# Optimization experiments

Hardware: AMD Instinct MI355X
Metric: run time of the kernel (lower is better)

## Reference

```python
import jax, jax.numpy as jnp
import numpy as np

B, NPG, K, H, G, L = 8, 128, 64, 600, 50, 6
N = B * NPG
CUTOFF = 10.0
BOX = 20.0
NUM_Z = 100


def setup_inputs() -> dict:
    key = jax.random.key(0)
    ks = jax.random.split(key, 16)
    s = 0.05
    z = jax.random.randint(ks[0], (N,), 0, 85)
    pos = jax.random.uniform(ks[1], (N, 3), dtype=jnp.float32) * BOX
    # weights stored as [in, out] (transposed torch Linear) so x @ w applies directly
    inp = {
        "z": z,
        "pos": pos,
        "embedding": jax.random.normal(ks[2], (NUM_Z, H), jnp.float32) * s,
        "mlp_w1": jax.random.normal(ks[3], (L, G, H), jnp.float32) * s,
        "mlp_b1": jnp.zeros((L, H), jnp.float32),
        "mlp_w2": jax.random.normal(ks[4], (L, H, H), jnp.float32) * s,
        "mlp_b2": jnp.zeros((L, H), jnp.float32),
        "lin1_w": jax.random.normal(ks[5], (L, H, H), jnp.float32) * s,  # CFConv lin1, no bias
        "lin2_w": jax.random.normal(ks[6], (L, H, H), jnp.float32) * s,
        "lin2_b": jnp.zeros((L, H), jnp.float32),
        "int_lin_w": jax.random.normal(ks[7], (L, H, H), jnp.float32) * s,
        "int_lin_b": jnp.zeros((L, H), jnp.float32),
        "pool_w": jax.random.normal(ks[8], (H, H), jnp.float32) * s,
        "pool_b": jnp.zeros((H,), jnp.float32),
    }
    return inp


def _ssp(x):
    # shifted softplus used by SchNet
    return jax.nn.softplus(x) - jnp.log(2.0)


def _build_graph(pos):
    # radius graph within each of the B graphs, capped at K neighbors per node
    posg = pos.reshape(B, NPG, 3)
    diff = posg[:, :, None, :] - posg[:, None, :, :]          # [B,n,n,3]
    dist2 = jnp.sum(diff * diff, axis=-1)                     # [B,n,n]
    eye = jnp.eye(NPG, dtype=bool)
    ok = (dist2 <= CUTOFF * CUTOFF) & (~eye)[None]
    neg = jnp.where(ok, -dist2, -jnp.inf)
    vals, idx = jax.lax.top_k(neg, K)                         # nearest K in-radius
    valid = jnp.isfinite(vals)                                # [B,n,K]
    nbr = idx + (jnp.arange(B) * NPG)[:, None, None]          # global node ids
    # recompute distances from gathered positions (differentiable, safe at masked slots)
    pos_nbr = pos[nbr.reshape(-1)].reshape(B, NPG, K, 3)
    dvec = posg[:, :, None, :] - pos_nbr
    dsq = jnp.sum(dvec * dvec, axis=-1)
    d = jnp.sqrt(jnp.where(valid, dsq, 1.0))
    d = jnp.where(valid, d, 0.0)                              # [B,n,K]
    return nbr, d, valid.astype(pos.dtype)


def reference(pos, embedding, mlp_w1, mlp_b1, mlp_w2, mlp_b2, lin1_w, lin2_w,
              lin2_b, int_lin_w, int_lin_b, pool_w, pool_b, z):
    nbr, d, valid = _build_graph(pos)
    nbr_flat = nbr.reshape(-1)

    # Gaussian smearing
    offs = jnp.linspace(0.0, CUTOFF, G)
    coeff = -0.5 / (offs[1] - offs[0]) ** 2
    edge_attr = jnp.exp(coeff * (d[..., None] - offs) ** 2)   # [B,n,K,G]
    # cosine cutoff, zero for invalid (padded) edges
    C = 0.5 * (jnp.cos(d * jnp.pi / CUTOFF) + 1.0) * valid    # [B,n,K]

    h = embedding[z]                                          # [N,H]
    for l in range(L):
        Wf = _ssp(edge_attr @ mlp_w1[l] + mlp_b1[l]) @ mlp_w2[l] + mlp_b2[l]
        Wf = Wf * C[..., None]                                # [B,n,K,H]
        x1 = h @ lin1_w[l]                                    # [N,H]
        xj = x1[nbr_flat].reshape(B, NPG, K, H)               # gather neighbors
        msg = jnp.sum(xj * Wf, axis=2).reshape(N, H)          # aggregate (add)
        m = msg @ lin2_w[l] + lin2_b[l]
        m = _ssp(m)
        m = m @ int_lin_w[l] + int_lin_b[l]
        h = h + m

    pooled = h.reshape(B, NPG, H).mean(axis=1)                # mean pool per graph
    return pooled @ pool_w + pool_b                           # [B, emb_dim]
```

## Files before the change

### kernel.cpp

```cpp
#include <hip/hip_runtime.h>
#include <cmath>

#define NB   8
#define NPG  128
#define NN   1024
#define KNB  64
#define HD   600
#define GG   50
#define LL   6
#define WROW 640
#define WCOL 640
#define NKNOT 1024

typedef __attribute__((ext_vector_type(8))) short short8;
typedef __attribute__((ext_vector_type(4))) float f32x4;

#define GLOAD16(gsrc, ldst) \
  __builtin_amdgcn_global_load_lds( \
      (const __attribute__((address_space(1))) void*)(gsrc), \
      (__attribute__((address_space(3))) void*)(ldst), 16, 0, 0)

__device__ __forceinline__ short f2b(float f) {
  union { float f; unsigned u; } v; v.f = f;
  unsigned u = v.u;
  u += 0x7fffu + ((u >> 16) & 1u);
  return (short)(u >> 16);
}

__device__ __forceinline__ float b2f(unsigned us) {
  union { unsigned u; float f; } v; v.u = us << 16; return v.f;
}

__device__ __forceinline__ float ssp_fast(float x) {
  return fmaxf(x, 0.0f) + __logf(1.0f + __expf(-fabsf(x))) - 0.69314718055994531f;
}

__global__ __launch_bounds__(256) void prolog_k(
    const float* __restrict__ pos, int* __restrict__ nbr,
    float* __restrict__ dist, float* __restrict__ cval,
    const float* __restrict__ w1, short* __restrict__ basis, short* __restrict__ w1b,
    const float* __restrict__ l1w, const float* __restrict__ l2w,
    const float* __restrict__ ilw, const float* __restrict__ w2,
    short* __restrict__ nwall,
    const int* __restrict__ z, const float* __restrict__ emb,
    float* __restrict__ h, short* __restrict__ hb, float* __restrict__ pooled) {
  int bid = blockIdx.x;
  int tid = threadIdx.x;
  if (bid < 512) {
#pragma clang fp contract(off)
    __shared__ float d2s[2][128];
    __shared__ int scnt[2];
    int sub = tid >> 7;
    int j = tid & 127;
    int i = bid*2 + sub;
    int li = i & 127;
    int base = i - li;
    if (j == 0) scnt[sub] = 0;
    float px = pos[3*i], py = pos[3*i+1], pz = pos[3*i+2];
    int gj = base + j;
    float dx = px - pos[3*gj], dy = py - pos[3*gj+1], dz = pz - pos[3*gj+2];
    float d2 = dx*dx + dy*dy + dz*dz;
    bool valid = (j != li) && (d2 <= 100.0f);
    d2s[sub][j] = valid ? d2 : 3.0e38f;
    __syncthreads();
    if (valid) {
      atomicAdd(&scnt[sub], 1);
      int rank = 0;
      for (int j2 = 0; j2 < 128; ++j2) {
        float o = d2s[sub][j2];
        rank += (o < d2 || (o == d2 && j2 < j)) ? 1 : 0;
      }
      if (rank < KNB) {
        int e = i*KNB + rank;
        nbr[e] = gj;
        float d = sqrtf(d2);
        dist[e] = d;
        cval[e] = 0.5f * (cosf(d * 0.31415926535897931f) + 1.0f);
      }
    }
    __syncthreads();
    int cnt = scnt[sub]; if (cnt > KNB) cnt = KNB;
    if (j < KNB && j >= cnt) {
      int e = i*KNB + j;
      nbr[e] = i; dist[e] = 0.0f; cval[e] = 0.0f;
    }
  } else if (bid < 1728) {
    int idx = (bid - 512)*256 + tid;
    if (idx < NKNOT*64) {
      int i = idx >> 6, g = idx & 63;
      float v = 0.0f;
      if (g < GG) {
        const float step = 10.0f/49.0f;
        const float coeff = -0.5f/(step*step);
        float d = (float)i * (10.0f/(float)(NKNOT-1));
        float dd = d - step*(float)g;
        v = __expf(coeff*dd*dd);
      }
      basis[idx] = f2b(v);
    } else {
      int r = idx - NKNOT*64;
      if (r < LL*WROW*64) {
        int l = r / (WROW*64); int rem = r - l*WROW*64;
        int n = rem >> 6, k = rem & 63;
        float v = (n < HD && k < GG) ? w1[(size_t)l*GG*HD + (size_t)k*HD + n] : 0.0f;
        w1b[r] = f2b(v);
      }
    }
  } else if (bid < 4128) {
    __shared__ float T[64][65];
    int r = bid - 1728;
    int w = r / 100; int rem = r - w*100;
    int ny = rem / 10, nz = rem - ny*10;
    int kind = w / 6, l = w - kind*6;
    const float* s = (kind == 0) ? l1w : (kind == 1) ? l2w : (kind == 2) ? ilw : w2;
    s += (size_t)l*360000;
    int n0 = ny*64, k0 = nz*64;
    int ta = tid & 63, tb = tid >> 6;
    #pragma unroll
    for (int p = 0; p < 16; ++p) {
      int k = k0 + p*4 + tb;
      int n = n0 + ta;
      T[p*4 + tb][ta] = (k < HD && n < HD) ? s[(size_t)k*HD + n] : 0.0f;
    }
    __syncthreads();
    #pragma unroll
    for (int p = 0; p < 16; ++p) {
      int n = n0 + p*4 + tb;
      int k = k0 + ta;
      if (k < WCOL)
        nwall[(size_t)w*WROW*WCOL + (size_t)n*WCOL + k] = f2b(T[ta][p*4 + tb]);
    }
  } else {
    int i = bid - 4128;
    int zi = z[i];
    for (int j = tid; j < WCOL; j += 256) {
      float v = (j < HD) ? emb[(size_t)zi*HD + j] : 0.0f;
      if (j < HD) h[(size_t)i*HD + j] = v;
      hb[(size_t)i*WCOL + j] = f2b(v);
    }
    if (i < NB) {
      for (int c = tid; c < HD; c += 256) pooled[(size_t)i*HD + c] = 0.0f;
    }
  }
}

__global__ __launch_bounds__(256) void tabA_k(const short* __restrict__ basis,
    const short* __restrict__ w1b, const float* __restrict__ b1all,
    short* __restrict__ ttab_all) {
  const int MT = NKNOT/128;
  int l = blockIdx.x / MT;
  int mb = blockIdx.x - l*MT;
  const short* Bw = w1b + (size_t)l*WROW*64;
  short* outb = ttab_all + (size_t)l*NKNOT*WCOL;
  __shared__ __align__(16) short As[128*40];
  __shared__ __align__(16) short Bs[128*40];
  int tid = threadIdx.x;
  int lane = tid & 63, wv = tid >> 6;
  int wr = wv >> 1, wc = wv & 1;
  int col = lane & 15, quad = lane >> 4;
  int m0 = mb * 128;
  int n0 = blockIdx.y * 128;
  f32x4 acc[4][4] = {};
  for (int k0 = 0; k0 < 64; k0 += 32) {
    #pragma unroll
    for (int rep = 0; rep < 2; ++rep) {
      int s = tid + rep*256;
      int row = s >> 2, seg = s & 3;
      *(short8*)&As[row*40 + seg*8] =
          *(const short8*)(basis + (size_t)(m0 + row)*64 + k0 + seg*8);
      *(short8*)&Bs[row*40 + seg*8] =
          *(const short8*)(Bw + (size_t)(n0 + row)*64 + k0 + seg*8);
    }
    __syncthreads();
    short8 af[4], bf[4];
    #pragma unroll
    for (int mt = 0; mt < 4; ++mt)
      af[mt] = *(const short8*)&As[(wr*64 + mt*16 + col)*40 + quad*8];
    #pragma unroll
    for (int jt = 0; jt < 4; ++jt)
      bf[jt] = *(const short8*)&Bs[(wc*64 + jt*16 + col)*40 + quad*8];
    #pragma unroll
    for (int mt = 0; mt < 4; ++mt)
      #pragma unroll
      for (int jt = 0; jt < 4; ++jt)
        acc[mt][jt] = __builtin_amdgcn_mfma_f32_16x16x32_bf16(af[mt], bf[jt], acc[mt][jt], 0, 0, 0);
    __syncthreads();
  }
  #pragma unroll
  for (int jt = 0; jt < 4; ++jt) {
    int j = n0 + wc*64 + jt*16 + col;
    if (j >= WCOL) continue;
    float bj = (j < HD) ? b1all[(size_t)l*HD + j] : 0.0f;
    #pragma unroll
    for (int mt = 0; mt < 4; ++mt)
      #pragma unroll
      for (int r = 0; r < 4; ++r) {
        int row = m0 + wr*64 + mt*16 + quad*4 + r;
        short v = (j < HD) ? f2b(ssp_fast(acc[mt][jt][r] + bj)) : (short)0;
        outb[(size_t)row*WCOL + j] = v;
      }
  }
}

__global__ __launch_bounds__(256) void tabB_k(const short* __restrict__ ttab_all,
    const short* __restrict__ nwall, const float* __restrict__ b2all,
    short* __restrict__ wtab_b) {
  const int MT = NKNOT/128;
  int l = blockIdx.x / MT;
  int mb = blockIdx.x - l*MT;
  const short* A  = ttab_all + (size_t)l*NKNOT*WCOL;
  const short* Bw = nwall + (size_t)(18 + l)*WROW*WCOL;
  short* P = wtab_b + (size_t)l*NKNOT*HD;
  __shared__ __align__(16) short As[128*40];
  __shared__ __align__(16) short Bs[128*40];
  int tid = threadIdx.x;
  int lane = tid & 63, wv = tid >> 6;
  int wr = wv >> 1, wc = wv & 1;
  int col = lane & 15, quad = lane >> 4;
  int m0 = mb * 128;
  int n0 = blockIdx.y * 128;
  f32x4 acc[4][4] = {};
  for (int k0 = 0; k0 < WCOL; k0 += 32) {
    #pragma unroll
    for (int rep = 0; rep < 2; ++rep) {
      int s = tid + rep*256;
      int row = s >> 2, seg = s & 3;
      *(short8*)&As[row*40 + seg*8] =
          *(const short8*)(A + (size_t)(m0 + row)*WCOL + k0 + seg*8);
      *(short8*)&Bs[row*40 + seg*8] =
          *(const short8*)(Bw + (size_t)(n0 + row)*WCOL + k0 + seg*8);
    }
    __syncthreads();
    short8 af[4], bf[4];
    #pragma unroll
    for (int mt = 0; mt < 4; ++mt)
      af[mt] = *(const short8*)&As[(wr*64 + mt*16 + col)*40 + quad*8];
    #pragma unroll
    for (int jt = 0; jt < 4; ++jt)
      bf[jt] = *(const short8*)&Bs[(wc*64 + jt*16 + col)*40 + quad*8];
    #pragma unroll
    for (int mt = 0; mt < 4; ++mt)
      #pragma unroll
      for (int jt = 0; jt < 4; ++jt)
        acc[mt][jt] = __builtin_amdgcn_mfma_f32_16x16x32_bf16(af[mt], bf[jt], acc[mt][jt], 0, 0, 0);
    __syncthreads();
  }
  #pragma unroll
  for (int jt = 0; jt < 4; ++jt) {
    int j = n0 + wc*64 + jt*16 + col;
    if (j >= HD) continue;
    float bj = b2all[(size_t)l*HD + j];
    #pragma unroll
    for (int mt = 0; mt < 4; ++mt)
      #pragma unroll
      for (int r = 0; r < 4; ++r) {
        int row = m0 + wr*64 + mt*16 + quad*4 + r;
        P[(size_t)row*HD + j] = f2b(acc[mt][jt][r] + bj);
      }
  }
}

__global__ __launch_bounds__(320) void gather_k(const short* __restrict__ tabb,
    const float* __restrict__ cval, const int* __restrict__ nbr,
    const float* __restrict__ dist, const short* __restrict__ x1b,
    short* __restrict__ msgb) {
  __shared__ float cvs[64];
  __shared__ int nbs[64];
  __shared__ int tix[64];
  __shared__ float tfr[64];
  int node = blockIdx.x, tid = threadIdx.x;
  if (tid < 64) {
    int e = node*KNB + tid;
    cvs[tid] = cval[e];
    nbs[tid] = nbr[e];
    float u = dist[e] * ((float)(NKNOT-1)/10.0f);
    int i = (int)u;
    if (i > NKNOT-2) i = NKNOT-2;
    tix[tid] = i;
    tfr[tid] = u - (float)i;
  }
  __syncthreads();
  int j = tid*2;
  if (j >= HD) {
    *(unsigned*)&msgb[(size_t)node*WCOL + j] = 0u;
    return;
  }
  float s0 = 0.f, s1 = 0.f;
  #pragma unroll 4
  for (int e = 0; e < KNB; ++e) {
    float Ce = cvs[e];
    if (Ce == 0.0f) continue;
    const short* w0 = tabb + (size_t)tix[e]*HD + j;
    float f = tfr[e];
    unsigned wa = *(const unsigned*)w0;
    unsigned wb = *(const unsigned*)(w0 + HD);
    unsigned xv = *(const unsigned*)(x1b + (size_t)nbs[e]*WCOL + j);
    float a0 = b2f(wa & 0xffffu), a1 = b2f(wa >> 16);
    float b0 = b2f(wb & 0xffffu), b1 = b2f(wb >> 16);
    float x0 = b2f(xv & 0xffffu), x1v = b2f(xv >> 16);
    s0 += Ce * (a0 + f*(b0 - a0)) * x0;
    s1 += Ce * (a1 + f*(b1 - a1)) * x1v;
  }
  unsigned pack = (unsigned)(unsigned short)f2b(s0) |
                  ((unsigned)(unsigned short)f2b(s1) << 16);
  *(unsigned*)&msgb[(size_t)node*WCOL + j] = pack;
}

template<int MODE>
__global__ __launch_bounds__(512) void gemm_node_k(
    const short* __restrict__ A, const short* __restrict__ Bw,
    const float* __restrict__ bias,
    short* __restrict__ outb, float* __restrict__ hacc, float* __restrict__ pooled) {
  __shared__ __align__(16) short As[2][2][32*64];
  __shared__ __align__(16) short Bs[2][2][64*64];
  __shared__ __align__(16) float red[2][256*8];
  int tid = threadIdx.x;
  int g = tid >> 8;
  int t = tid & 255;
  int lane = t & 63, wv = t >> 6;
  int col = lane & 15, quad = lane >> 4;
  int m0 = blockIdx.x * 32;
  int n0 = blockIdx.y * 64;
  const int kb = g * 320;
  int a_gi = wv*64 + lane;
  int a_row = a_gi >> 3;
  int a_gc = (a_gi & 7) ^ (a_row & 7);
  const short* a_src = A + (size_t)(m0 + a_row)*WCOL + kb + a_gc*8;
  int b_gi0 = wv*128 + lane;
  int b_row0 = b_gi0 >> 3;
  int b_gc0 = (b_gi0 & 7) ^ (b_row0 & 7);
  const short* b_src0 = Bw + (size_t)(n0 + b_row0)*WCOL + kb + b_gc0*8;
  int b_gi1 = b_gi0 + 64;
  int b_row1 = b_gi1 >> 3;
  int b_gc1 = (b_gi1 & 7) ^ (b_row1 & 7);
  const short* b_src1 = Bw + (size_t)(n0 + b_row1)*WCOL + kb + b_gc1*8;
  short* a_dst[2]  = { &As[g][0][a_gi*8],  &As[g][1][a_gi*8] };
  short* b_dst0[2] = { &Bs[g][0][b_gi0*8], &Bs[g][1][b_gi0*8] };
  short* b_dst1[2] = { &Bs[g][0][b_gi1*8], &Bs[g][1][b_gi1*8] };
  GLOAD16(a_src, a_dst[0]);
  GLOAD16(b_src0, b_dst0[0]);
  GLOAD16(b_src1, b_dst1[0]);
  __syncthreads();
  f32x4 acc[2] = {};
  #pragma unroll
  for (int kk = 0; kk < 5; ++kk) {
    const int cur = kk & 1, nxt = cur ^ 1;
    if (kk < 4) {
      GLOAD16(a_src + (kk+1)*64, a_dst[nxt]);
      GLOAD16(b_src0 + (kk+1)*64, b_dst0[nxt]);
      GLOAD16(b_src1 + (kk+1)*64, b_dst1[nxt]);
    }
    #pragma unroll
    for (int kh = 0; kh < 2; ++kh) {
      int brow = wv*16 + col;
      int bgr = brow*8 + ((kh*4 + quad) ^ (brow & 7));
      short8 bf = *(const short8*)&Bs[g][cur][bgr*8];
      #pragma unroll
      for (int mt = 0; mt < 2; ++mt) {
        int arow = mt*16 + col;
        int agr = arow*8 + ((kh*4 + quad) ^ (arow & 7));
        short8 af = *(const short8*)&As[g][cur][agr*8];
        acc[mt] = __builtin_amdgcn_mfma_f32_16x16x32_bf16(af, bf, acc[mt], 0, 0, 0);
      }
    }
    __syncthreads();
  }
  #pragma unroll
  for (int mt = 0; mt < 2; ++mt)
    *(f32x4*)&red[g][(t*2 + mt)*4] = acc[mt];
  __syncthreads();
  const int mt = g;
  f32x4 v = *(const f32x4*)&red[0][(t*2 + mt)*4];
  v += *(const f32x4*)&red[1][(t*2 + mt)*4];
  int j = n0 + wv*16 + col;
  if (MODE == 0) {
    #pragma unroll
    for (int r = 0; r < 4; ++r) {
      int row = m0 + mt*16 + quad*4 + r;
      outb[(size_t)row*WCOL + j] = (j < HD) ? f2b(v[r]) : (short)0;
    }
  } else if (MODE == 1) {
    float bj = (j < HD) ? bias[j] : 0.0f;
    #pragma unroll
    for (int r = 0; r < 4; ++r) {
      int row = m0 + mt*16 + quad*4 + r;
      outb[(size_t)row*WCOL + j] = (j < HD) ? f2b(ssp_fast(v[r] + bj)) : (short)0;
    }
  } else {
    float psum = 0.0f;
    #pragma unroll
    for (int r = 0; r < 4; ++r) {
      int row = m0 + mt*16 + quad*4 + r;
      if (j < HD) {
        float nv = hacc[(size_t)row*HD + j] + v[r] + bias[j];
        hacc[(size_t)row*HD + j] = nv;
        outb[(size_t)row*WCOL + j] = f2b(nv);
        psum += nv;
      } else {
        outb[(size_t)row*WCOL + j] = 0;
      }
    }
    if (MODE == 3 && j < HD) {
      int b = m0 >> 7;
      atomicAdd(&pooled[(size_t)b*HD + j], psum * (1.0f/128.0f));
    }
  }
}

__global__ __launch_bounds__(256) void pool_out_k(const float* __restrict__ pooled,
    const float* __restrict__ pw, const float* __restrict__ pb,
    float* __restrict__ out) {
  __shared__ float red[4][64];
  int b = blockIdx.y;
  int tid = threadIdx.x;
  int jl = tid & 63, q = tid >> 6;
  int j = blockIdx.x*64 + jl;
  float s = 0.0f;
  if (j < HD) {
    int c0 = q*150, c1 = c0 + 150;
    for (int c = c0; c < c1; ++c)
      s += pooled[(size_t)b*HD + c] * pw[(size_t)c*HD + j];
  }
  red[q][jl] = s;
  __syncthreads();
  if (q == 0 && j < HD)
    out[(size_t)b*HD + j] = red[0][jl] + red[1][jl] + red[2][jl] + red[3][jl] + pb[j];
}

extern "C" void kernel_launch(void* const* d_in, const int* in_sizes, int n_in,
                              void* d_out, int out_size, void* d_ws, size_t ws_size,
                              hipStream_t stream) {
  const int*   z    = (const int*)d_in[0];
  const float* pos  = (const float*)d_in[1];
  const float* emb  = (const float*)d_in[2];
  const float* w1   = (const float*)d_in[3];
  const float* b1   = (const float*)d_in[4];
  const float* w2   = (const float*)d_in[5];
  const float* b2   = (const float*)d_in[6];
  const float* l1w  = (const float*)d_in[7];
  const float* l2w  = (const float*)d_in[8];
  const float* l2b  = (const float*)d_in[9];
  const float* ilw  = (const float*)d_in[10];
  const float* ilb  = (const float*)d_in[11];
  const float* pw   = (const float*)d_in[12];
  const float* pb   = (const float*)d_in[13];
  float* ws = (float*)d_ws;
  int*   nbr   = (int*)ws;
  float* cv    = ws + 65536;
  float* dist  = ws + 131072;
  float* pooled= ws + 196608;
  float* h     = ws + 204800;
  short* h_b   = (short*)(ws + 819200);
  short* msg_b = (short*)(ws + 1146880);
  short* mtmp_b= (short*)(ws + 1474560);
  short* x1_b  = (short*)(ws + 1802240);
  short* basis = (short*)(ws + 2129920);
  short* ttab  = (short*)(ws + 2162688);
  short* wtab_b= (short*)(ws + 4128768);
  short* w1b   = (short*)(ws + 5971968);
  short* nwall = (short*)(ws + 6094848);
  float* out   = (float*)d_out;

  const size_t WSZ = (size_t)WROW*WCOL;

  prolog_k<<<5152, 256, 0, stream>>>(pos, nbr, dist, cv,
      w1, basis, w1b, l1w, l2w, ilw, w2, nwall, z, emb, h, h_b, pooled);
  tabA_k<<<dim3(LL*(NKNOT/128), 5), 256, 0, stream>>>(basis, w1b, b1, ttab);
  tabB_k<<<dim3(LL*(NKNOT/128), 5), 256, 0, stream>>>(ttab, nwall, b2, wtab_b);

  dim3 gn(32, 10);
  for (int l = 0; l < LL; ++l) {
    gemm_node_k<0><<<gn, 512, 0, stream>>>(h_b, nwall + (size_t)(0*6 + l)*WSZ,
        nullptr, x1_b, nullptr, nullptr);
    gather_k<<<NN, 320, 0, stream>>>(wtab_b + (size_t)l*NKNOT*HD, cv, nbr, dist, x1_b, msg_b);
    gemm_node_k<1><<<gn, 512, 0, stream>>>(msg_b, nwall + (size_t)(1*6 + l)*WSZ,
        l2b + (size_t)l*HD, mtmp_b, nullptr, nullptr);
    if (l < LL-1)
      gemm_node_k<2><<<gn, 512, 0, stream>>>(mtmp_b, nwall + (size_t)(2*6 + l)*WSZ,
          ilb + (size_t)l*HD, h_b, h, nullptr);
    else
      gemm_node_k<3><<<gn, 512, 0, stream>>>(mtmp_b, nwall + (size_t)(2*6 + l)*WSZ,
          ilb + (size_t)l*HD, h_b, h, pooled);
  }
  pool_out_k<<<dim3(10, NB), 256, 0, stream>>>(pooled, pw, pb, out);
}
```

Measured before the change: 408.6 us.

## Double-buffer tabB GEMM tiles via direct global-to-LDS loads with XOR swizzle

The table-building GEMM kernel now stages its A and B tiles with asynchronous global_load_lds into two LDS buffers. The next K-slice is prefetched while MFMAs run on the current one, which is meant to hide global load latency behind compute. Padded rows are replaced by an XOR-swizzled 32-short layout to avoid LDS bank conflicts without the padding. This doubles LDS use and relies on correct wait/barrier placement for the async copies.

```diff
diff --git a/kernel.cpp b/kernel.cpp
--- a/kernel.cpp
+++ b/kernel.cpp
@@ -211,33 +211,49 @@
   const short* A  = ttab_all + (size_t)l*NKNOT*WCOL;
   const short* Bw = nwall + (size_t)(18 + l)*WROW*WCOL;
   short* P = wtab_b + (size_t)l*NKNOT*HD;
-  __shared__ __align__(16) short As[128*40];
-  __shared__ __align__(16) short Bs[128*40];
+  __shared__ __align__(16) short As[2][128*32];
+  __shared__ __align__(16) short Bs[2][128*32];
   int tid = threadIdx.x;
   int lane = tid & 63, wv = tid >> 6;
   int wr = wv >> 1, wc = wv & 1;
   int col = lane & 15, quad = lane >> 4;
   int m0 = mb * 128;
   int n0 = blockIdx.y * 128;
+  int g0 = tid, g1 = tid + 256;
+  int r0 = g0 >> 2, s0 = (g0 & 3) ^ (r0 & 3);
+  int r1 = g1 >> 2, s1 = (g1 & 3) ^ (r1 & 3);
+  const short* a_s0 = A  + (size_t)(m0 + r0)*WCOL + s0*8;
+  const short* a_s1 = A  + (size_t)(m0 + r1)*WCOL + s1*8;
+  const short* b_s0 = Bw + (size_t)(n0 + r0)*WCOL + s0*8;
+  const short* b_s1 = Bw + (size_t)(n0 + r1)*WCOL + s1*8;
+  GLOAD16(a_s0, &As[0][g0*8]);
+  GLOAD16(a_s1, &As[0][g1*8]);
+  GLOAD16(b_s0, &Bs[0][g0*8]);
+  GLOAD16(b_s1, &Bs[0][g1*8]);
+  __syncthreads();
   f32x4 acc[4][4] = {};
-  for (int k0 = 0; k0 < WCOL; k0 += 32) {
-    #pragma unroll
-    for (int rep = 0; rep < 2; ++rep) {
-      int s = tid + rep*256;
-      int row = s >> 2, seg = s & 3;
-      *(short8*)&As[row*40 + seg*8] =
-          *(const short8*)(A + (size_t)(m0 + row)*WCOL + k0 + seg*8);
-      *(short8*)&Bs[row*40 + seg*8] =
-          *(const short8*)(Bw + (size_t)(n0 + row)*WCOL + k0 + seg*8);
-    }
-    __syncthreads();
+  for (int kk = 0; kk < 20; ++kk) {
+    int cur = kk & 1, nxt = cur ^ 1;
+    if (kk < 19) {
+      int k0 = (kk + 1)*32;
+      GLOAD16(a_s0 + k0, &As[nxt][g0*8]);
+      GLOAD16(a_s1 + k0, &As[nxt][g1*8]);
+      GLOAD16(b_s0 + k0, &Bs[nxt][g0*8]);
+      GLOAD16(b_s1 + k0, &Bs[nxt][g1*8]);
+    }
     short8 af[4], bf[4];
     #pragma unroll
-    for (int mt = 0; mt < 4; ++mt)
-      af[mt] = *(const short8*)&As[(wr*64 + mt*16 + col)*40 + quad*8];
-    #pragma unroll
-    for (int jt = 0; jt < 4; ++jt)
-      bf[jt] = *(const short8*)&Bs[(wc*64 + jt*16 + col)*40 + quad*8];
+    for (int mt = 0; mt < 4; ++mt) {
+      int ar = wr*64 + mt*16 + col;
+      int agr = ar*4 + (quad ^ (ar & 3));
+      af[mt] = *(const short8*)&As[cur][agr*8];
+    }
+    #pragma unroll
+    for (int jt = 0; jt < 4; ++jt) {
+      int br = wc*64 + jt*16 + col;
+      int bgr = br*4 + (quad ^ (br & 3));
+      bf[jt] = *(const short8*)&Bs[cur][bgr*8];
+    }
     #pragma unroll
     for (int mt = 0; mt < 4; ++mt)
       #pragma unroll
```

After: 411.0 us. Within noise of the previous version (+0.6%).
